# Performance work log

Measured on AMD Instinct MI355X. Metric: run time of the kernel, lower is better.

The kernel has to match this reference:

```python
import jax, jax.numpy as jnp
import numpy as np

N, D_IN, UNITS = 8192, 4096, 4096

def setup_inputs() -> dict:
    key = jax.random.key(0)
    k1, k2 = jax.random.split(key)
    x = jax.random.normal(k1, (N, D_IN), dtype=jnp.float32)
    # weight initialized RandomNormal(stddev=0.1) in the original build()
    w = jax.random.normal(k2, (D_IN, UNITS), dtype=jnp.float32) * 0.1
    return {"x": x, "w": w}

def reference(x, w):
    # BinaryDense: sign-binarize both activations and weights, then dense matmul.
    # tf.sign semantics: sign(0) == 0, matched by jnp.sign.
    x_bin = jnp.sign(x)  # [N, d_in]
    w_bin = jnp.sign(w)  # [d_in, units]
    return jnp.matmul(x_bin, w_bin)  # [N, units]
```

## Files before the change

kernel.cpp:

```cpp
#include <hip/hip_runtime.h>
#include <stdint.h>

#define M_DIM 8192
#define K_DIM 4096
#define N_DIM 4096
#define KB (K_DIM / 2)

typedef unsigned char u8;
typedef unsigned int u32;
typedef int i32x4 __attribute__((ext_vector_type(4)));
typedef int i32x8 __attribute__((ext_vector_type(8)));
typedef float f32x4 __attribute__((ext_vector_type(4)));
typedef float float4v __attribute__((ext_vector_type(4)));
typedef u32 u32x2 __attribute__((ext_vector_type(2)));

__device__ __forceinline__ u32 sign_fp4(float v) {
  return v > 0.0f ? 0x2u : (v < 0.0f ? 0xAu : 0x0u);
}

__device__ __forceinline__ u32 pk16(u32 v) {
  return (v & 0xFu) | ((v >> 4) & 0xF0u) | ((v >> 8) & 0xF00u) | ((v >> 12) & 0xF000u);
}

__global__ void binarize_fused(const float* __restrict__ x, const float* __restrict__ w,
                               u32* __restrict__ xb, u8* __restrict__ wT) {
  const int tid = threadIdx.x;
  const int bid = blockIdx.x;
  const int r3 = bid % 3;
  if (r3 != 2) {
    __shared__ u8 tile[64][68];
    const int wtile = (bid / 3) * 2 + r3;
    const int bn = (wtile & 63) * 64;
    const int bk = (wtile >> 6) * 64;

#pragma unroll
    for (int it = 0; it < 4; ++it) {
      int idx = tid + it * 256;
      int rr = idx >> 4;
      int c = (idx & 15) * 4;
      float4v v = *(const float4v*)&w[(size_t)(bk + rr) * N_DIM + bn + c];
      tile[c + 0][rr] = (u8)sign_fp4(v.x);
      tile[c + 1][rr] = (u8)sign_fp4(v.y);
      tile[c + 2][rr] = (u8)sign_fp4(v.z);
      tile[c + 3][rr] = (u8)sign_fp4(v.w);
    }
    __syncthreads();
    const int rn = tid >> 2;
    const int cbyte = (tid & 3) * 8;
    const u32* trow = (const u32*)&tile[rn][0];
    u32 q0 = trow[cbyte / 2 + 0];
    u32 q1 = trow[cbyte / 2 + 1];
    u32 q2 = trow[cbyte / 2 + 2];
    u32 q3 = trow[cbyte / 2 + 3];
    u32x2 o;
    o.x = pk16(q0) | (pk16(q1) << 16);
    o.y = pk16(q2) | (pk16(q3) << 16);
    *(u32x2*)&wT[(size_t)(bn + rn) * KB + (bk >> 1) + cbyte] = o;
  } else {
    const int n8 = M_DIM * K_DIM / 8;
    int i = (bid / 3) * 256 + tid;
    const int stride = 2048 * 256;
    for (; i < n8; i += stride) {
      float4v v0 = ((const float4v*)x)[2 * i];
      float4v v1 = ((const float4v*)x)[2 * i + 1];
      u32 wd = sign_fp4(v0.x) | (sign_fp4(v0.y) << 4) | (sign_fp4(v0.z) << 8) |
               (sign_fp4(v0.w) << 12) | (sign_fp4(v1.x) << 16) | (sign_fp4(v1.y) << 20) |
               (sign_fp4(v1.z) << 24) | (sign_fp4(v1.w) << 28);
      xb[i] = wd;
    }
  }
}

#define BM 256
#define BN 256
#define BKB 128
#define NT (K_DIM / 256)

__device__ __forceinline__ void gload_lds16(const u8* g, u8* l) {
  __builtin_amdgcn_global_load_lds(
      (const __attribute__((address_space(1))) void*)g,
      (__attribute__((address_space(3))) void*)l, 16, 0, 0);
}

__device__ __forceinline__ i32x8 pad8(i32x4 v) {
  return __builtin_shufflevector(v, v, 0, 1, 2, 3, -1, -1, -1, -1);
}

__device__ __forceinline__ f32x4 mfma_fp4(i32x4 a, i32x4 b, f32x4 c) {
  return __builtin_amdgcn_mfma_scale_f32_16x16x128_f8f6f4(pad8(a), pad8(b), c, 4, 4, 0, 0x7F, 0,
                                                          0x7F);
}

__global__ __launch_bounds__(512, 2) void gemm_bin_fp4(const u8* __restrict__ A,
                                                       const u8* __restrict__ Bt,
                                                       float* __restrict__ C) {
  __shared__ u8 lds[2][4][128 * 128];

  const int tid = threadIdx.x;
  const int lane = tid & 63;
  const int wid = tid >> 6;
  const int wr = wid >> 2;
  const int wc = wid & 3;

  const int b = blockIdx.x;
  const int sw = (b & 7) * (gridDim.x >> 3) + (b >> 3);
  const int tiles_n = N_DIM / BN;
  const int bm = (sw / tiles_n) * BM;
  const int bn = (sw % tiles_n) * BN;

  const int l15 = lane & 15;
  const int g4 = lane >> 4;
  const int srow = lane >> 3;
  const int swz_src = (((lane & 7) ^ srow) << 4);

  auto stage = [&](int buf, int slot, const u8* gbase) {
#pragma unroll
    for (int i = 0; i < 2; ++i) {
      const u8* g = gbase + (size_t)(i * 64 + wid * 8 + srow) * KB + swz_src;
      gload_lds16(g, &lds[buf][slot][(i * 64 + wid * 8) * 128]);
    }
  };

  f32x4 acc[8][4] = {};

  {
    const u8* Abase = A + (size_t)bm * KB;
    const u8* Bbase = Bt + (size_t)bn * KB;
    stage(0, 0, Abase);
    stage(0, 1, Abase + (size_t)128 * KB);
    stage(0, 2, Bbase);
    stage(0, 3, Bbase + (size_t)128 * KB);
    stage(1, 2, Bbase + BKB);
    stage(1, 3, Bbase + (size_t)128 * KB + BKB);
  }
  asm volatile("s_waitcnt vmcnt(4)" ::: "memory");
  __builtin_amdgcn_s_barrier();

  for (int t = 0; t < NT; ++t) {
    const int buf = t & 1;
    const u8* As = &lds[buf][wr][0];
    const u8* Bs = &lds[buf][2 + (wc >> 1)][0];
    const int brow0 = (wc & 1) * 64;
    const u8* Anext = A + (size_t)bm * KB + (t + 1) * BKB;
    const u8* Bnext2 = Bt + (size_t)bn * KB + (t + 2) * BKB;

    i32x4 a0[4], a1[4], a2[4], a3[4], b0[4], b1[4];

#pragma unroll
    for (int m = 0; m < 4; ++m) {
      int row = m * 16 + l15;
      int col = (g4 * 16) ^ ((row & 7) << 4);
      a0[m] = *(const i32x4*)&As[row * 128 + col];
    }
#pragma unroll
    for (int n = 0; n < 4; ++n) {
      int row = brow0 + n * 16 + l15;
      int col = (g4 * 16) ^ ((row & 7) << 4);
      b0[n] = *(const i32x4*)&Bs[row * 128 + col];
    }
    if (t + 1 < NT) {
      stage(buf ^ 1, 0, Anext);
      stage(buf ^ 1, 1, Anext + (size_t)128 * KB);
    }
    __builtin_amdgcn_sched_barrier(0);

#pragma unroll
    for (int m = 0; m < 4; ++m) {
      int row = m * 16 + l15;
      int col = (64 + g4 * 16) ^ ((row & 7) << 4);
      a1[m] = *(const i32x4*)&As[row * 128 + col];
    }
#pragma unroll
    for (int n = 0; n < 4; ++n) {
      int row = brow0 + n * 16 + l15;
      int col = (64 + g4 * 16) ^ ((row & 7) << 4);
      b1[n] = *(const i32x4*)&Bs[row * 128 + col];
    }
    __builtin_amdgcn_sched_barrier(0);

    __builtin_amdgcn_s_setprio(1);
#pragma unroll
    for (int m = 0; m < 4; ++m)
#pragma unroll
      for (int n = 0; n < 4; ++n)
        acc[m][n] = mfma_fp4(a0[m], b0[n], acc[m][n]);
    __builtin_amdgcn_s_setprio(0);
    __builtin_amdgcn_sched_barrier(0);

#pragma unroll
    for (int m = 0; m < 4; ++m) {
      int row = 64 + m * 16 + l15;
      int col = (g4 * 16) ^ ((row & 7) << 4);
      a2[m] = *(const i32x4*)&As[row * 128 + col];
    }
#pragma unroll
    for (int m = 0; m < 4; ++m) {
      int row = 64 + m * 16 + l15;
      int col = (64 + g4 * 16) ^ ((row & 7) << 4);
      a3[m] = *(const i32x4*)&As[row * 128 + col];
    }
    __builtin_amdgcn_sched_barrier(0);

    __builtin_amdgcn_s_setprio(1);
#pragma unroll
    for (int m = 0; m < 4; ++m)
#pragma unroll
      for (int n = 0; n < 4; ++n)
        acc[m][n] = mfma_fp4(a1[m], b1[n], acc[m][n]);
    __builtin_amdgcn_s_setprio(0);

    __builtin_amdgcn_s_barrier();

    if (t + 2 < NT) {
      stage(buf, 2, Bnext2);
      stage(buf, 3, Bnext2 + (size_t)128 * KB);
    }
    __builtin_amdgcn_sched_barrier(0);

    __builtin_amdgcn_s_setprio(1);
#pragma unroll
    for (int m = 0; m < 4; ++m)
#pragma unroll
      for (int n = 0; n < 4; ++n)
        acc[4 + m][n] = mfma_fp4(a2[m], b0[n], acc[4 + m][n]);
    __builtin_amdgcn_s_setprio(0);
    __builtin_amdgcn_sched_barrier(0);

    __builtin_amdgcn_s_setprio(1);
#pragma unroll
    for (int m = 0; m < 4; ++m)
#pragma unroll
      for (int n = 0; n < 4; ++n)
        acc[4 + m][n] = mfma_fp4(a3[m], b1[n], acc[4 + m][n]);
    __builtin_amdgcn_s_setprio(0);

    if (t + 2 < NT)
      asm volatile("s_waitcnt vmcnt(4)" ::: "memory");
    else
      asm volatile("s_waitcnt vmcnt(0)" ::: "memory");
    __builtin_amdgcn_s_barrier();
  }

  const int crow0 = bm + wr * 128;
  const int ccol0 = bn + wc * 64;
#pragma unroll
  for (int m = 0; m < 8; ++m)
#pragma unroll
    for (int n = 0; n < 4; ++n)
#pragma unroll
      for (int j = 0; j < 4; ++j)
        C[(size_t)(crow0 + m * 16 + g4 * 4 + j) * N_DIM + ccol0 + n * 16 + l15] = acc[m][n][j];
}

__global__ void naive_bin_gemm(const float* __restrict__ X, const float* __restrict__ W,
                               float* __restrict__ C) {
  int j = blockIdx.x * blockDim.x + threadIdx.x;
  int i = blockIdx.y;
  if (j >= N_DIM) return;
  float s = 0.0f;
  for (int k = 0; k < K_DIM; ++k) {
    float xv = X[(size_t)i * K_DIM + k];
    float wv = W[(size_t)k * N_DIM + j];
    float sx = (float)((xv > 0.0f) - (xv < 0.0f));
    float sw = (float)((wv > 0.0f) - (wv < 0.0f));
    s += sx * sw;
  }
  C[(size_t)i * N_DIM + j] = s;
}

extern "C" void kernel_launch(void* const* d_in, const int* in_sizes, int n_in,
                              void* d_out, int out_size, void* d_ws, size_t ws_size,
                              hipStream_t stream) {
  const float* x = (const float*)d_in[0];
  const float* w = (const float*)d_in[1];
  float* out = (float*)d_out;

  const size_t xb_bytes = (size_t)M_DIM * KB;
  const size_t wt_bytes = (size_t)N_DIM * KB;

  if (ws_size >= xb_bytes + wt_bytes) {
    u8* xb = (u8*)d_ws;
    u8* wt = (u8*)((char*)d_ws + xb_bytes);

    binarize_fused<<<6144, 256, 0, stream>>>(x, w, (u32*)xb, wt);

    const int grid = (M_DIM / BM) * (N_DIM / BN);
    gemm_bin_fp4<<<grid, 512, 0, stream>>>(xb, wt, out);
  } else {
    naive_bin_gemm<<<dim3(N_DIM / 256, M_DIM), dim3(256), 0, stream>>>(x, w, out);
  }
}
```

Measured before the change: 125.8 us.

## Prefetch next tile's first LDS fragments and rebalance waitcnt placement

The first-k-half A/B fragments (a0/b0) of the next K tile are now read from the other LDS buffer at the end of the current iteration, overlapping with the last MFMA block. The a3 read moves after the mid-iteration barrier, and the global-load wait becomes a full vmcnt(0) before that barrier instead of a partial wait at the end. The aim is to hide LDS read latency at the start of each iteration. The cost is that the current iteration must wait earlier for its in-flight A tile loads, which may expose global memory latency.

New measurement: 125.7 us. About the same (-0.0%).

```diff
diff --git a/kernel.cpp b/kernel.cpp
--- a/kernel.cpp
+++ b/kernel.cpp
@@ -91,8 +91,8 @@
                                                           0x7F);
 }
 
-__global__ __launch_bounds__(512, 2) void gemm_bin_fp4(const u8* __restrict__ A,
-                                                       const u8* __restrict__ Bt,
+__global__ __launch_bounds__(512, 2) void gemm_bin_fp4(const u8* __restrict__ Ag,
+                                                       const u8* __restrict__ Btg,
                                                        float* __restrict__ C) {
   __shared__ u8 lds[2][4][128 * 128];
 
@@ -110,6 +110,7 @@
 
   const int l15 = lane & 15;
   const int g4 = lane >> 4;
+  const int brow0 = (wc & 1) * 64;
   const int srow = lane >> 3;
   const int swz_src = (((lane & 7) ^ srow) << 4);
 
@@ -124,8 +125,8 @@
   f32x4 acc[8][4] = {};
 
   {
-    const u8* Abase = A + (size_t)bm * KB;
-    const u8* Bbase = Bt + (size_t)bn * KB;
+    const u8* Abase = Ag + (size_t)bm * KB;
+    const u8* Bbase = Btg + (size_t)bn * KB;
     stage(0, 0, Abase);
     stage(0, 1, Abase + (size_t)128 * KB);
     stage(0, 2, Bbase);
@@ -136,45 +137,45 @@
   asm volatile("s_waitcnt vmcnt(4)" ::: "memory");
   __builtin_amdgcn_s_barrier();
 
+  i32x4 a0[4], b0[4];
+  {
+    const u8* As0 = &lds[0][wr][0];
+    const u8* Bs0 = &lds[0][2 + (wc >> 1)][0];
+#pragma unroll
+    for (int m = 0; m < 4; ++m) {
+      int row = m * 16 + l15;
+      a0[m] = *(const i32x4*)&As0[row * 128 + ((g4 * 16) ^ ((row & 7) << 4))];
+    }
+#pragma unroll
+    for (int n = 0; n < 4; ++n) {
+      int row = brow0 + n * 16 + l15;
+      b0[n] = *(const i32x4*)&Bs0[row * 128 + ((g4 * 16) ^ ((row & 7) << 4))];
+    }
+  }
+
   for (int t = 0; t < NT; ++t) {
     const int buf = t & 1;
     const u8* As = &lds[buf][wr][0];
     const u8* Bs = &lds[buf][2 + (wc >> 1)][0];
-    const int brow0 = (wc & 1) * 64;
-    const u8* Anext = A + (size_t)bm * KB + (t + 1) * BKB;
-    const u8* Bnext2 = Bt + (size_t)bn * KB + (t + 2) * BKB;
-
-    i32x4 a0[4], a1[4], a2[4], a3[4], b0[4], b1[4];
+    const u8* AsN = &lds[buf ^ 1][wr][0];
+    const u8* BsN = &lds[buf ^ 1][2 + (wc >> 1)][0];
+
+    i32x4 a1[4], a2[4], a3[4], b1[4];
 
 #pragma unroll
     for (int m = 0; m < 4; ++m) {
       int row = m * 16 + l15;
-      int col = (g4 * 16) ^ ((row & 7) << 4);
-      a0[m] = *(const i32x4*)&As[row * 128 + col];
+      a1[m] = *(const i32x4*)&As[row * 128 + ((64 + g4 * 16) ^ ((row & 7) << 4))];
     }
 #pragma unroll
     for (int n = 0; n < 4; ++n) {
       int row = brow0 + n * 16 + l15;
-      int col = (g4 * 16) ^ ((row & 7) << 4);
-      b0[n] = *(const i32x4*)&Bs[row * 128 + col];
+      b1[n] = *(const i32x4*)&Bs[row * 128 + ((64 + g4 * 16) ^ ((row & 7) << 4))];
     }
     if (t + 1 < NT) {
-      stage(buf ^ 1, 0, Anext);
-      stage(buf ^ 1, 1, Anext + (size_t)128 * KB);
-    }
-    __builtin_amdgcn_sched_barrier(0);
-
-#pragma unroll
-    for (int m = 0; m < 4; ++m) {
-      int row = m * 16 + l15;
-      int col = (64 + g4 * 16) ^ ((row & 7) << 4);
-      a1[m] = *(const i32x4*)&As[row * 128 + col];
-    }
-#pragma unroll
-    for (int n = 0; n < 4; ++n) {
-      int row = brow0 + n * 16 + l15;
-      int col = (64 + g4 * 16) ^ ((row & 7) << 4);
-      b1[n] = *(const i32x4*)&Bs[row * 128 + col];
+      const u8* An = Ag + (size_t)bm * KB + (t + 1) * BKB;
+      stage(buf ^ 1, 0, An);
+      stage(buf ^ 1, 1, An + (size_t)128 * KB);
     }
     __builtin_amdgcn_sched_barrier(0);
 
@@ -190,14 +191,7 @@
 #pragma unroll
     for (int m = 0; m < 4; ++m) {
       int row = 64 + m * 16 + l15;
-      int col = (g4 * 16) ^ ((row & 7) << 4);
-      a2[m] = *(const i32x4*)&As[row * 128 + col];
-    }
-#pragma unroll
-    for (int m = 0; m < 4; ++m) {
-      int row = 64 + m * 16 + l15;
-      int col = (64 + g4 * 16) ^ ((row & 7) << 4);
-      a3[m] = *(const i32x4*)&As[row * 128 + col];
+      a2[m] = *(const i32x4*)&As[row * 128 + ((g4 * 16) ^ ((row & 7) << 4))];
     }
     __builtin_amdgcn_sched_barrier(0);
 
@@ -209,11 +203,18 @@
         acc[m][n] = mfma_fp4(a1[m], b1[n], acc[m][n]);
     __builtin_amdgcn_s_setprio(0);
 
+    asm volatile("s_waitcnt vmcnt(0)" ::: "memory");
     __builtin_amdgcn_s_barrier();
 
     if (t + 2 < NT) {
-      stage(buf, 2, Bnext2);
-      stage(buf, 3, Bnext2 + (size_t)128 * KB);
+      const u8* Bn = Btg + (size_t)bn * KB + (t + 2) * BKB;
+      stage(buf, 2, Bn);
+      stage(buf, 3, Bn + (size_t)128 * KB);
+    }
+#pragma unroll
+    for (int m = 0; m < 4; ++m) {
+      int row = 64 + m * 16 + l15;
+      a3[m] = *(const i32x4*)&As[row * 128 + ((64 + g4 * 16) ^ ((row & 7) << 4))];
     }
     __builtin_amdgcn_sched_barrier(0);
 
@@ -226,6 +227,20 @@
     __builtin_amdgcn_s_setprio(0);
     __builtin_amdgcn_sched_barrier(0);
 
+    if (t + 1 < NT) {
+#pragma unroll
+      for (int m = 0; m < 4; ++m) {
+        int row = m * 16 + l15;
+        a0[m] = *(const i32x4*)&AsN[row * 128 + ((g4 * 16) ^ ((row & 7) << 4))];
+      }
+#pragma unroll
+      for (int n = 0; n < 4; ++n) {
+        int row = brow0 + n * 16 + l15;
+        b0[n] = *(const i32x4*)&BsN[row * 128 + ((g4 * 16) ^ ((row & 7) << 4))];
+      }
+    }
+    __builtin_amdgcn_sched_barrier(0);
+
     __builtin_amdgcn_s_setprio(1);
 #pragma unroll
     for (int m = 0; m < 4; ++m)
@@ -234,10 +249,6 @@
         acc[4 + m][n] = mfma_fp4(a3[m], b1[n], acc[4 + m][n]);
     __builtin_amdgcn_s_setprio(0);
 
-    if (t + 2 < NT)
-      asm volatile("s_waitcnt vmcnt(4)" ::: "memory");
-    else
-      asm volatile("s_waitcnt vmcnt(0)" ::: "memory");
     __builtin_amdgcn_s_barrier();
   }
 
```

## Replace double-buffered 256x256 GEMM with single-buffered 128x128 tiles

Applied to the files above, without the earlier changes.

The fp4 MFMA GEMM drops from 512-thread 256x256 tiles with a double-buffered, prefetching, priority-scheduled pipeline to 256-thread 128x128 tiles. Each K step now loads into one LDS buffer, waits for all loads, then computes. This cuts LDS and register use per block so more blocks fit per CU. In exchange it loses load/compute overlap and doubles global reads of both operands.

Result: slower. 167.3 us (+33.0%).

```diff
diff --git a/kernel.cpp b/kernel.cpp
--- a/kernel.cpp
+++ b/kernel.cpp
@@ -71,8 +71,8 @@
   }
 }
 
-#define BM 256
-#define BN 256
+#define BM 128
+#define BN 128
 #define BKB 128
 #define NT (K_DIM / 256)
 
@@ -91,16 +91,17 @@
                                                           0x7F);
 }
 
-__global__ __launch_bounds__(512, 2) void gemm_bin_fp4(const u8* __restrict__ A,
-                                                       const u8* __restrict__ Bt,
+__global__ __launch_bounds__(256, 4) void gemm_bin_fp4(const u8* __restrict__ Ag,
+                                                       const u8* __restrict__ Btg,
                                                        float* __restrict__ C) {
-  __shared__ u8 lds[2][4][128 * 128];
+  __shared__ u8 As[128 * 128];
+  __shared__ u8 Bs[128 * 128];
 
   const int tid = threadIdx.x;
   const int lane = tid & 63;
   const int wid = tid >> 6;
-  const int wr = wid >> 2;
-  const int wc = wid & 3;
+  const int wr = wid >> 1;
+  const int wc = wid & 1;
 
   const int b = blockIdx.x;
   const int sw = (b & 7) * (gridDim.x >> 3) + (b >> 3);
@@ -113,138 +114,50 @@
   const int srow = lane >> 3;
   const int swz_src = (((lane & 7) ^ srow) << 4);
 
-  auto stage = [&](int buf, int slot, const u8* gbase) {
-#pragma unroll
-    for (int i = 0; i < 2; ++i) {
-      const u8* g = gbase + (size_t)(i * 64 + wid * 8 + srow) * KB + swz_src;
-      gload_lds16(g, &lds[buf][slot][(i * 64 + wid * 8) * 128]);
-    }
-  };
-
-  f32x4 acc[8][4] = {};
-
-  {
-    const u8* Abase = A + (size_t)bm * KB;
-    const u8* Bbase = Bt + (size_t)bn * KB;
-    stage(0, 0, Abase);
-    stage(0, 1, Abase + (size_t)128 * KB);
-    stage(0, 2, Bbase);
-    stage(0, 3, Bbase + (size_t)128 * KB);
-    stage(1, 2, Bbase + BKB);
-    stage(1, 3, Bbase + (size_t)128 * KB + BKB);
-  }
-  asm volatile("s_waitcnt vmcnt(4)" ::: "memory");
-  __builtin_amdgcn_s_barrier();
+  const u8* Abase = Ag + (size_t)bm * KB;
+  const u8* Bbase = Btg + (size_t)bn * KB;
+
+  f32x4 acc[4][4] = {};
 
   for (int t = 0; t < NT; ++t) {
-    const int buf = t & 1;
-    const u8* As = &lds[buf][wr][0];
-    const u8* Bs = &lds[buf][2 + (wc >> 1)][0];
-    const int brow0 = (wc & 1) * 64;
-    const u8* Anext = A + (size_t)bm * KB + (t + 1) * BKB;
-    const u8* Bnext2 = Bt + (size_t)bn * KB + (t + 2) * BKB;
-
-    i32x4 a0[4], a1[4], a2[4], a3[4], b0[4], b1[4];
-
-#pragma unroll
-    for (int m = 0; m < 4; ++m) {
-      int row = m * 16 + l15;
-      int col = (g4 * 16) ^ ((row & 7) << 4);
-      a0[m] = *(const i32x4*)&As[row * 128 + col];
-    }
-#pragma unroll
-    for (int n = 0; n < 4; ++n) {
-      int row = brow0 + n * 16 + l15;
-      int col = (g4 * 16) ^ ((row & 7) << 4);
-      b0[n] = *(const i32x4*)&Bs[row * 128 + col];
-    }
-    if (t + 1 < NT) {
-      stage(buf ^ 1, 0, Anext);
-      stage(buf ^ 1, 1, Anext + (size_t)128 * KB);
-    }
-    __builtin_amdgcn_sched_barrier(0);
-
-#pragma unroll
-    for (int m = 0; m < 4; ++m) {
-      int row = m * 16 + l15;
-      int col = (64 + g4 * 16) ^ ((row & 7) << 4);
-      a1[m] = *(const i32x4*)&As[row * 128 + col];
-    }
-#pragma unroll
-    for (int n = 0; n < 4; ++n) {
-      int row = brow0 + n * 16 + l15;
-      int col = (64 + g4 * 16) ^ ((row & 7) << 4);
-      b1[n] = *(const i32x4*)&Bs[row * 128 + col];
-    }
-    __builtin_amdgcn_sched_barrier(0);
-
-    __builtin_amdgcn_s_setprio(1);
-#pragma unroll
-    for (int m = 0; m < 4; ++m)
-#pragma unroll
-      for (int n = 0; n < 4; ++n)
-        acc[m][n] = mfma_fp4(a0[m], b0[n], acc[m][n]);
-    __builtin_amdgcn_s_setprio(0);
-    __builtin_amdgcn_sched_barrier(0);
-
-#pragma unroll
-    for (int m = 0; m < 4; ++m) {
-      int row = 64 + m * 16 + l15;
-      int col = (g4 * 16) ^ ((row & 7) << 4);
-      a2[m] = *(const i32x4*)&As[row * 128 + col];
-    }
-#pragma unroll
-    for (int m = 0; m < 4; ++m) {
-      int row = 64 + m * 16 + l15;
-      int col = (64 + g4 * 16) ^ ((row & 7) << 4);
-      a3[m] = *(const i32x4*)&As[row * 128 + col];
-    }
-    __builtin_amdgcn_sched_barrier(0);
-
-    __builtin_amdgcn_s_setprio(1);
-#pragma unroll
-    for (int m = 0; m < 4; ++m)
-#pragma unroll
-      for (int n = 0; n < 4; ++n)
-        acc[m][n] = mfma_fp4(a1[m], b1[n], acc[m][n]);
-    __builtin_amdgcn_s_setprio(0);
-
+    const int kt = t * BKB;
+#pragma unroll
+    for (int i = 0; i < 4; ++i) {
+      const int row = wid * 32 + i * 8 + srow;
+      gload_lds16(Abase + (size_t)row * KB + kt + swz_src, &As[(wid * 32 + i * 8) * 128]);
+      gload_lds16(Bbase + (size_t)row * KB + kt + swz_src, &Bs[(wid * 32 + i * 8) * 128]);
+    }
+    asm volatile("s_waitcnt vmcnt(0)" ::: "memory");
     __builtin_amdgcn_s_barrier();
 
-    if (t + 2 < NT) {
-      stage(buf, 2, Bnext2);
-      stage(buf, 3, Bnext2 + (size_t)128 * KB);
-    }
-    __builtin_amdgcn_sched_barrier(0);
-
-    __builtin_amdgcn_s_setprio(1);
-#pragma unroll
-    for (int m = 0; m < 4; ++m)
-#pragma unroll
-      for (int n = 0; n < 4; ++n)
-        acc[4 + m][n] = mfma_fp4(a2[m], b0[n], acc[4 + m][n]);
-    __builtin_amdgcn_s_setprio(0);
-    __builtin_amdgcn_sched_barrier(0);
-
-    __builtin_amdgcn_s_setprio(1);
-#pragma unroll
-    for (int m = 0; m < 4; ++m)
-#pragma unroll
-      for (int n = 0; n < 4; ++n)
-        acc[4 + m][n] = mfma_fp4(a3[m], b1[n], acc[4 + m][n]);
-    __builtin_amdgcn_s_setprio(0);
-
-    if (t + 2 < NT)
-      asm volatile("s_waitcnt vmcnt(4)" ::: "memory");
-    else
-      asm volatile("s_waitcnt vmcnt(0)" ::: "memory");
+#pragma unroll
+    for (int kk = 0; kk < 2; ++kk) {
+      i32x4 af[4], bf[4];
+#pragma unroll
+      for (int m = 0; m < 4; ++m) {
+        int row = wr * 64 + m * 16 + l15;
+        int col = (kk * 64 + g4 * 16) ^ ((row & 7) << 4);
+        af[m] = *(const i32x4*)&As[row * 128 + col];
+      }
+#pragma unroll
+      for (int n = 0; n < 4; ++n) {
+        int row = wc * 64 + n * 16 + l15;
+        int col = (kk * 64 + g4 * 16) ^ ((row & 7) << 4);
+        bf[n] = *(const i32x4*)&Bs[row * 128 + col];
+      }
+#pragma unroll
+      for (int m = 0; m < 4; ++m)
+#pragma unroll
+        for (int n = 0; n < 4; ++n)
+          acc[m][n] = mfma_fp4(af[m], bf[n], acc[m][n]);
+    }
     __builtin_amdgcn_s_barrier();
   }
 
-  const int crow0 = bm + wr * 128;
+  const int crow0 = bm + wr * 64;
   const int ccol0 = bn + wc * 64;
 #pragma unroll
-  for (int m = 0; m < 8; ++m)
+  for (int m = 0; m < 4; ++m)
 #pragma unroll
     for (int n = 0; n < 4; ++n)
 #pragma unroll
@@ -285,7 +198,7 @@
     binarize_fused<<<6144, 256, 0, stream>>>(x, w, (u32*)xb, wt);
 
     const int grid = (M_DIM / BM) * (N_DIM / BN);
-    gemm_bin_fp4<<<grid, 512, 0, stream>>>(xb, wt, out);
+    gemm_bin_fp4<<<grid, 256, 0, stream>>>(xb, wt, out);
   } else {
     naive_bin_gemm<<<dim3(N_DIM / 256, M_DIM), dim3(256), 0, stream>>>(x, w, out);
   }
```
